# Performance work log

Hardware: AMD Instinct MI355X
Metric: run time of the kernel (lower is better)

Reference implementation:

```python
import jax, jax.numpy as jnp
import numpy as np

H = 0.5  # Parzen window bandwidth


def setup_inputs() -> dict:
    key = jax.random.key(0)
    k1, k2 = jax.random.split(key)
    test_Xs = jax.random.normal(k1, (1024, 32), dtype=jnp.float32)
    train_Xs = jax.random.normal(k2, (4096, 32), dtype=jnp.float32)
    return {"test_Xs": test_Xs, "train_Xs": train_Xs}


def reference(test_Xs, train_Xs):
    # test_Xs: [N, d], train_Xs: [M, d]
    dim = test_Xs.shape[1]
    # broadcast pairwise differences: [N, M, d]
    diffs = test_Xs[:, None, :] - train_Xs[None, :, :]
    # point is inside the window iff |diff|/h <= 0.5 along every dim
    n_inside = jnp.all(jnp.abs(diffs) / H <= 0.5, axis=2)  # [N, M] bool
    coef = 1.0 / H ** dim
    return jnp.mean(coef * n_inside.astype(test_Xs.dtype), axis=1)  # [N]
```

## Files before the change

### kernel.cpp

```cpp
#include <hip/hip_runtime.h>
#include <math.h>


__global__ __launch_bounds__(256)
void parzen_init(float* __restrict__ out, int n) {
    int i = blockIdx.x * 256 + threadIdx.x;
    if (i < n) out[i] = 0.0f;
}

__global__ __launch_bounds__(256)
void parzen_main(const float* __restrict__ test_Xs,
                 const float* __restrict__ train_Xs,
                 float* __restrict__ out,
                 int M, int nchunk, int mchunk, float scale) {
    const int lane = threadIdx.x & 63;
    const int wave = threadIdx.x >> 6;
    const int g    = blockIdx.x / nchunk;
    const int c    = blockIdx.x % nchunk;
    const int n    = g * 64 + lane;

    float4 t[8];
    const float4* tp = reinterpret_cast<const float4*>(test_Xs + (size_t)n * 32);
#pragma unroll
    for (int q = 0; q < 8; ++q) t[q] = tp[q];

    const int per_wave = mchunk >> 2;
    const int m0 = c * mchunk + wave * per_wave;
    const int m1 = (m0 + per_wave < M) ? (m0 + per_wave) : M;

    int count = 0;
    for (int m = m0; m < m1; ++m) {
        const float4* xp = reinterpret_cast<const float4*>(train_Xs + (size_t)m * 32);
        bool in = true;
#pragma unroll
        for (int q = 0; q < 8; ++q) {
            const float4 x  = xp[q];
            const float4 tg = t[q];
            in = in & (fabsf(tg.x - x.x) <= 0.25f)
                    & (fabsf(tg.y - x.y) <= 0.25f)
                    & (fabsf(tg.z - x.z) <= 0.25f)
                    & (fabsf(tg.w - x.w) <= 0.25f);
        }
        count += in ? 1 : 0;
    }

    __shared__ int cnt[4][64];
    cnt[wave][lane] = count;
    __syncthreads();
    if (wave == 0) {
        int s = cnt[0][lane] + cnt[1][lane] + cnt[2][lane] + cnt[3][lane];
        if (s) atomicAdd(&out[n], (float)s * scale);
    }
}

extern "C" void kernel_launch(void* const* d_in, const int* in_sizes, int n_in,
                              void* d_out, int out_size, void* d_ws, size_t ws_size,
                              hipStream_t stream) {
    const float* test_Xs  = (const float*)d_in[0];
    const float* train_Xs = (const float*)d_in[1];
    float* out = (float*)d_out;

    const int N = in_sizes[0] / 32;
    const int M = in_sizes[1] / 32;

    const float scale = (float)(4294967296.0 / (double)M);

    parzen_init<<<(out_size + 255) / 256, 256, 0, stream>>>(out, out_size);

    const int mchunk = 128;
    const int nchunk = (M + mchunk - 1) / mchunk;
    const int ngroup = N / 64;
    parzen_main<<<ngroup * nchunk, 256, 0, stream>>>(
        test_Xs, train_Xs, out, M, nchunk, mchunk, scale);
}
```

Measured before the change: 75.10 us.

## Replace atomics with workspace partial counts and a separate reduce kernel

The init kernel and the float atomicAdd are replaced by per-chunk integer counts written to a workspace, followed by a second kernel that sums over chunks and scales. The M chunk is halved to double the grid size, the loop is unrolled by 4, and the per-element compare-and-AND test is replaced by two fmax accumulators that are compared once against the threshold. This aims to raise occupancy and cut ALU work per pair. The cost is a second launch plus workspace traffic, and the result depends on d_ws being large enough.

```diff
diff --git a/kernel.cpp b/kernel.cpp
--- a/kernel.cpp
+++ b/kernel.cpp
@@ -2,17 +2,14 @@
 #include <math.h>
 
 
-__global__ __launch_bounds__(256)
-void parzen_init(float* __restrict__ out, int n) {
-    int i = blockIdx.x * 256 + threadIdx.x;
-    if (i < n) out[i] = 0.0f;
-}
+#define MCHUNK 64
+#define WAVES  4
 
 __global__ __launch_bounds__(256)
-void parzen_main(const float* __restrict__ test_Xs,
-                 const float* __restrict__ train_Xs,
-                 float* __restrict__ out,
-                 int M, int nchunk, int mchunk, float scale) {
+void parzen_partial(const float* __restrict__ test_Xs,
+                    const float* __restrict__ train_Xs,
+                    int* __restrict__ ws,
+                    int M, int N, int nchunk) {
     const int lane = threadIdx.x & 63;
     const int wave = threadIdx.x >> 6;
     const int g    = blockIdx.x / nchunk;
@@ -24,33 +21,45 @@
 #pragma unroll
     for (int q = 0; q < 8; ++q) t[q] = tp[q];
 
-    const int per_wave = mchunk >> 2;
-    const int m0 = c * mchunk + wave * per_wave;
+    const int per_wave = MCHUNK / WAVES;
+    const int m0 = c * MCHUNK + wave * per_wave;
     const int m1 = (m0 + per_wave < M) ? (m0 + per_wave) : M;
 
     int count = 0;
+#pragma unroll 4
     for (int m = m0; m < m1; ++m) {
         const float4* xp = reinterpret_cast<const float4*>(train_Xs + (size_t)m * 32);
-        bool in = true;
+        float acc0 = 0.0f, acc1 = 0.0f;
 #pragma unroll
-        for (int q = 0; q < 8; ++q) {
-            const float4 x  = xp[q];
-            const float4 tg = t[q];
-            in = in & (fabsf(tg.x - x.x) <= 0.25f)
-                    & (fabsf(tg.y - x.y) <= 0.25f)
-                    & (fabsf(tg.z - x.z) <= 0.25f)
-                    & (fabsf(tg.w - x.w) <= 0.25f);
+        for (int q = 0; q < 8; q += 2) {
+            const float4 x0 = xp[q],   x1 = xp[q + 1];
+            const float4 t0 = t[q],    t1 = t[q + 1];
+            acc0 = fmaxf(fmaxf(acc0, fabsf(t0.x - x0.x)), fabsf(t0.y - x0.y));
+            acc0 = fmaxf(fmaxf(acc0, fabsf(t0.z - x0.z)), fabsf(t0.w - x0.w));
+            acc1 = fmaxf(fmaxf(acc1, fabsf(t1.x - x1.x)), fabsf(t1.y - x1.y));
+            acc1 = fmaxf(fmaxf(acc1, fabsf(t1.z - x1.z)), fabsf(t1.w - x1.w));
         }
-        count += in ? 1 : 0;
+        count += (fmaxf(acc0, acc1) <= 0.25f) ? 1 : 0;
     }
 
-    __shared__ int cnt[4][64];
+    __shared__ int cnt[WAVES][64];
     cnt[wave][lane] = count;
     __syncthreads();
     if (wave == 0) {
         int s = cnt[0][lane] + cnt[1][lane] + cnt[2][lane] + cnt[3][lane];
-        if (s) atomicAdd(&out[n], (float)s * scale);
+        ws[(size_t)c * N + n] = s;
     }
+}
+
+__global__ __launch_bounds__(256)
+void parzen_reduce(const int* __restrict__ ws, float* __restrict__ out,
+                   int N, int nchunk, float scale) {
+    const int n = blockIdx.x * 256 + threadIdx.x;
+    if (n >= N) return;
+    int s = 0;
+#pragma unroll 8
+    for (int c = 0; c < nchunk; ++c) s += ws[(size_t)c * N + n];
+    out[n] = (float)s * scale;
 }
 
 extern "C" void kernel_launch(void* const* d_in, const int* in_sizes, int n_in,
@@ -59,17 +68,17 @@
     const float* test_Xs  = (const float*)d_in[0];
     const float* train_Xs = (const float*)d_in[1];
     float* out = (float*)d_out;
+    int*   ws  = (int*)d_ws;
 
     const int N = in_sizes[0] / 32;
     const int M = in_sizes[1] / 32;
 
     const float scale = (float)(4294967296.0 / (double)M);
 
-    parzen_init<<<(out_size + 255) / 256, 256, 0, stream>>>(out, out_size);
-
-    const int mchunk = 128;
-    const int nchunk = (M + mchunk - 1) / mchunk;
+    const int nchunk = (M + MCHUNK - 1) / MCHUNK;
     const int ngroup = N / 64;
-    parzen_main<<<ngroup * nchunk, 256, 0, stream>>>(
-        test_Xs, train_Xs, out, M, nchunk, mchunk, scale);
+    parzen_partial<<<ngroup * nchunk, 256, 0, stream>>>(
+        test_Xs, train_Xs, ws, M, N, nchunk);
+    parzen_reduce<<<(N + 255) / 256, 256, 0, stream>>>(
+        ws, out, N, nchunk, scale);
 }
```

After: 80.25 us. 1.07x slower.
